# Kernel optimization log

Measured on AMD Instinct MI355X. Metric: run time of the kernel, lower is better.

Reference implementation:

```python
import jax, jax.numpy as jnp
import numpy as np

N_NODES = 80000
N_EDGES = 800000
N_REL = 400
D_IN = 256
D_OUT = 256
BN_EPS = 1e-5


def _xavier(key, shape, gain=np.sqrt(2.0)):
    fan_in, fan_out = shape[0], shape[-1]
    std = gain * np.sqrt(2.0 / (fan_in + fan_out))
    return jax.random.normal(key, shape, dtype=jnp.float32) * std


def ccorr(a, b):
    # circular correlation: irfft(conj(rfft(a)) * rfft(b), n)
    n = a.shape[-1]
    return jnp.fft.irfft(jnp.conj(jnp.fft.rfft(a)) * jnp.fft.rfft(b), n)


def setup_inputs() -> dict:
    key = jax.random.key(0)
    ks = jax.random.split(key, 12)
    x = jax.random.normal(ks[0], (N_NODES, D_IN), dtype=jnp.float32)
    rel_repr = jax.random.normal(ks[1], (N_REL, D_IN), dtype=jnp.float32)
    edge_src = jax.random.randint(ks[2], (N_EDGES,), 0, N_NODES)
    edge_dst = jax.random.randint(ks[3], (N_EDGES,), 0, N_NODES)
    edge_type = jax.random.randint(ks[4], (N_EDGES,), 0, N_REL)
    edge_norm = jax.random.uniform(ks[5], (N_EDGES,), dtype=jnp.float32)
    in_w = _xavier(ks[6], (D_IN, D_OUT))
    out_w = _xavier(ks[7], (D_IN, D_OUT))
    loop_w = _xavier(ks[8], (D_IN, D_OUT))
    w_rel = _xavier(ks[9], (D_IN, D_OUT))
    loop_rel = _xavier(ks[10], (1, D_IN))
    bias = jnp.zeros((D_OUT,), dtype=jnp.float32)
    return {"x": x, "rel_repr": rel_repr, "edge_src": edge_src,
            "edge_dst": edge_dst, "edge_type": edge_type, "edge_norm": edge_norm,
            "in_w": in_w, "out_w": out_w, "loop_w": loop_w, "w_rel": w_rel,
            "loop_rel": loop_rel, "bias": bias}


def reference(x, rel_repr, edge_src, edge_dst, edge_type, edge_norm,
              in_w, out_w, loop_w, w_rel, loop_rel, bias):
    E = edge_src.shape[0]
    half = E // 2
    # gather + compose (opn == 'corr')
    h_src = x[edge_src]                         # [E, D_in]
    edge_data = ccorr(h_src, rel_repr[edge_type])  # [E, D_in]
    # direction-split matmul
    msg = jnp.concatenate([edge_data[:half] @ in_w,
                           edge_data[half:] @ out_w], axis=0)  # [E, D_out]
    msg = msg * edge_norm[:, None]
    # scatter-sum into destination nodes, then reduce (dropout p=0, /3)
    agg = jax.ops.segment_sum(msg, edge_dst, num_segments=x.shape[0]) / 3.0
    # self-loop
    loop = ccorr(x, jnp.broadcast_to(loop_rel, x.shape)) @ loop_w / 3.0
    out = agg + loop + bias
    # BatchNorm1d (training mode: batch stats, gamma=1, beta=0)
    mean = jnp.mean(out, axis=0)
    var = jnp.var(out, axis=0)
    out = (out - mean) / jnp.sqrt(var + BN_EPS)
    # act is identity
    return out, rel_repr @ w_rel
```

## Files before the change

### kernel.cpp

```cpp
#include <hip/hip_runtime.h>

#define NN 80000
#define NE 800000
#define EH 400000
#define NR 400
#define DD 256
#define NFP 260
#define KT 772
#define KP 832
#define NB 160000
#define NCH 157
#define MT 80400
#define PI2 6.283185307179586f

typedef unsigned short u16;
typedef __attribute__((ext_vector_type(8))) short bf16x8;
typedef __attribute__((ext_vector_type(4))) float f32x4;

static __device__ __forceinline__ float bu2f(u16 u) {
  return __uint_as_float(((unsigned int)u) << 16);
}
static __device__ __forceinline__ u16 f2bu(float f) {
  unsigned int x = __float_as_uint(f);
  x += 0x7fffu + ((x >> 16) & 1u);
  return (u16)(x >> 16);
}
static __device__ __forceinline__ unsigned int pk2(float a, float b) {
  return (unsigned int)f2bu(a) | ((unsigned int)f2bu(b) << 16);
}
static __device__ __forceinline__ void gload16(const void* g, void* l) {
  __builtin_amdgcn_global_load_lds(
      (const __attribute__((address_space(1))) unsigned int*)g,
      (__attribute__((address_space(3))) unsigned int*)l, 16, 0, 0);
}

__global__ void k_build_f(u16* __restrict__ Ft) {
  int c = blockIdx.x, j = threadIdx.x;
  int k = c >> 1;
  int m = (j * k) & 255;
  float th = -PI2 * (float)m * (1.0f / 256.0f);
  float v = (c & 1) ? sinf(th) : cosf(th);
  Ft[c * 256 + j] = f2bu(v);
}

__global__ void k_build_m(const float* __restrict__ in_w, const float* __restrict__ out_w,
                          u16* __restrict__ Bt) {
  int t = blockIdx.x;
  int c = threadIdx.x;
  const float* W = (t < 258) ? in_w : out_w;
  int tp = (t < 258) ? t : t - 258;
  int k = tp >> 1, im = tp & 1;
  float a = (k == 0 || k == 128) ? 1.0f : 2.0f;
  float scale = a * (1.0f / (256.0f * 3.0f));
  float th = -PI2 * (float)k * (1.0f / 256.0f);
  float wr = cosf(th), wi = sinf(th);
  float zr = 1.0f, zi = 0.0f;
  float acc = 0.0f;
  for (int j = 0; j < DD; ++j) {
    float coef = im ? zi : zr;
    acc += coef * W[(size_t)j * DD + c];
    float nzr = zr * wr - zi * wi; zi = zr * wi + zi * wr; zr = nzr;
  }
  Bt[(size_t)c * KP + t] = f2bu(scale * acc);
}

__global__ void k_build_q(const float* __restrict__ lr, const float* __restrict__ loop_w,
                          u16* __restrict__ Bt) {
  __shared__ float L[DD];
  int j = blockIdx.x, c = threadIdx.x;
  L[c] = lr[c];
  __syncthreads();
  float acc = 0.0f;
  for (int k2 = 0; k2 < DD; ++k2)
    acc += L[(j + k2) & 255] * loop_w[(size_t)k2 * DD + c];
  Bt[(size_t)c * KP + 516 + j] = f2bu(acc * (1.0f / 3.0f));
  if (j < KP - KT) Bt[(size_t)c * KP + KT + j] = 0;
}

__global__ __launch_bounds__(256) void k_cvt(const float* __restrict__ x,
                                             u16* __restrict__ Ap, u16* __restrict__ xb,
                                             u16* __restrict__ xfh) {
  int w = threadIdx.x >> 6, lane = threadIdx.x & 63;
  size_t row = (size_t)blockIdx.x * 4 + w;
  float4 v = *(const float4*)(x + row * DD + 4 * lane);
  ushort4 pk;
  pk.x = f2bu(v.x); pk.y = f2bu(v.y); pk.z = f2bu(v.z); pk.w = f2bu(v.w);
  *(ushort4*)(xb + row * DD + 4 * lane) = pk;
  *(ushort4*)(Ap + row * KP + 516 + 4 * lane) = pk;
  if (lane < 15) *(uint2*)(Ap + row * KP + KT + 4 * lane) = make_uint2(0u, 0u);
  float s = v.x - v.y + v.z - v.w;
#pragma unroll
  for (int off = 32; off > 0; off >>= 1) s += __shfl_xor(s, off);
  if (lane == 0) {
    xfh[row * NFP + 256] = f2bu(s);
    xfh[row * NFP + 257] = 0;
  }
}

__global__ __launch_bounds__(256) void k_cvtr(const float* __restrict__ rel,
                                              u16* __restrict__ xb, u16* __restrict__ rfh) {
  int w = threadIdx.x >> 6, lane = threadIdx.x & 63;
  size_t row = (size_t)blockIdx.x * 4 + w;
  float4 v = *(const float4*)(rel + row * DD + 4 * lane);
  ushort4 pk;
  pk.x = f2bu(v.x); pk.y = f2bu(v.y); pk.z = f2bu(v.z); pk.w = f2bu(v.w);
  *(ushort4*)(xb + (NN + row) * DD + 4 * lane) = pk;
  float s = v.x - v.y + v.z - v.w;
#pragma unroll
  for (int off = 32; off > 0; off >>= 1) s += __shfl_xor(s, off);
  if (lane == 0) {
    rfh[row * NFP + 256] = f2bu(s);
    rfh[row * NFP + 257] = 0;
  }
}

__global__ __launch_bounds__(256) void k_dft(
    const u16* __restrict__ xb, const u16* __restrict__ Ft,
    u16* __restrict__ xfh, u16* __restrict__ rfh) {
  __shared__ u16 sA[128 * 64];
  __shared__ u16 sB[128 * 64];
  int tid = threadIdx.x;
  int mt0 = (int)(blockIdx.x >> 1) * 128;
  int nt0 = (blockIdx.x & 1) * 128;
  int w = tid >> 6, lane = tid & 63;
  int wm = (w & 1) * 64, wn = (w >> 1) * 64;
  int fr = lane & 15, fg = lane >> 4;
  int rbase = tid >> 3;
  int cbe = (tid & 7) * 8;
  int wadr = rbase * 64 + (cbe ^ ((rbase & 7) * 8));

  f32x4 acc[4][4];
#pragma unroll
  for (int i = 0; i < 4; ++i)
#pragma unroll
    for (int j = 0; j < 4; ++j) acc[i][j] = (f32x4){0.f, 0.f, 0.f, 0.f};

  bf16x8 ra[4], rb[4];
#define LOADT(kb)                                                                   \
  {                                                                                 \
    _Pragma("unroll") for (int q = 0; q < 4; ++q) {                                 \
      int rr = mt0 + rbase + q * 32; if (rr > MT - 1) rr = MT - 1;                  \
      ra[q] = *(const bf16x8*)(xb + (size_t)rr * DD + (kb) * 64 + cbe);             \
      rb[q] = *(const bf16x8*)(Ft + (size_t)(nt0 + rbase + q * 32) * DD + (kb) * 64 + cbe); \
    }                                                                               \
  }

  LOADT(0)
  for (int kb = 0; kb < 4; ++kb) {
    __syncthreads();
#pragma unroll
    for (int q = 0; q < 4; ++q) {
      *(bf16x8*)(sA + q * 2048 + wadr) = ra[q];
      *(bf16x8*)(sB + q * 2048 + wadr) = rb[q];
    }
    __syncthreads();
    if (kb + 1 < 4) LOADT(kb + 1)
#pragma unroll
    for (int ks = 0; ks < 2; ++ks) {
      bf16x8 af[4], bf_[4];
#pragma unroll
      for (int mt = 0; mt < 4; ++mt) {
        int r = wm + mt * 16 + fr;
        af[mt] = *(const bf16x8*)(sA + r * 64 + ((ks * 32 + fg * 8) ^ ((r & 7) * 8)));
      }
#pragma unroll
      for (int nt = 0; nt < 4; ++nt) {
        int r = wn + nt * 16 + fr;
        bf_[nt] = *(const bf16x8*)(sB + r * 64 + ((ks * 32 + fg * 8) ^ ((r & 7) * 8)));
      }
#pragma unroll
      for (int mt = 0; mt < 4; ++mt)
#pragma unroll
        for (int nt = 0; nt < 4; ++nt)
          acc[mt][nt] = __builtin_amdgcn_mfma_f32_16x16x32_bf16(af[mt], bf_[nt],
                                                                acc[mt][nt], 0, 0, 0);
    }
  }
#undef LOADT

#pragma unroll
  for (int mt = 0; mt < 4; ++mt)
#pragma unroll
    for (int nt = 0; nt < 4; ++nt) {
      int cg = nt0 + wn + nt * 16 + fr;
#pragma unroll
      for (int j = 0; j < 4; ++j) {
        int rg = mt0 + wm + mt * 16 + fg * 4 + j;
        u16 val = f2bu(acc[mt][nt][j]);
        if (rg < NN)      xfh[(size_t)rg * NFP + cg] = val;
        else if (rg < MT) rfh[(size_t)(rg - NN) * NFP + cg] = val;
      }
    }
}

__global__ void k_hist(const int* __restrict__ edst, int* __restrict__ cnt) {
  int e = blockIdx.x * 256 + threadIdx.x;
  int key = edst[e] + ((e >= EH) ? NN : 0);
  atomicAdd(&cnt[key], 1);
}

__global__ __launch_bounds__(256) void k_scan1(const int* __restrict__ cnt,
                                               int* __restrict__ base,
                                               int* __restrict__ chunkTot) {
  __shared__ int wsum[4];
  int t = threadIdx.x;
  int g0 = blockIdx.x * 1024 + t * 4;
  int v[4], ex[4], s = 0;
#pragma unroll
  for (int j = 0; j < 4; ++j) v[j] = (g0 + j < NB) ? cnt[g0 + j] : 0;
#pragma unroll
  for (int j = 0; j < 4; ++j) { ex[j] = s; s += v[j]; }
  int lane = t & 63, w = t >> 6;
  int inc = s;
  for (int off = 1; off < 64; off <<= 1) {
    int n = __shfl_up(inc, off);
    if (lane >= off) inc += n;
  }
  if (lane == 63) wsum[w] = inc;
  __syncthreads();
  int woff = 0;
  for (int i = 0; i < w; ++i) woff += wsum[i];
  int exth = woff + inc - s;
#pragma unroll
  for (int j = 0; j < 4; ++j)
    if (g0 + j < NB) base[g0 + j] = exth + ex[j];
  if (t == 255) chunkTot[blockIdx.x] = woff + inc;
}

__global__ __launch_bounds__(256) void k_scan2(const int* __restrict__ chunkTot,
                                               int* __restrict__ chunkOff) {
  __shared__ int wsum[4];
  int t = threadIdx.x;
  int v = (t < NCH) ? chunkTot[t] : 0;
  int lane = t & 63, w = t >> 6;
  int inc = v;
  for (int off = 1; off < 64; off <<= 1) {
    int n = __shfl_up(inc, off);
    if (lane >= off) inc += n;
  }
  if (lane == 63) wsum[w] = inc;
  __syncthreads();
  int woff = 0;
  for (int i = 0; i < w; ++i) woff += wsum[i];
  if (t < NCH) chunkOff[t] = woff + inc - v;
}

__global__ void k_scan3(int* __restrict__ base, const int* __restrict__ chunkOff,
                        int* __restrict__ cursor) {
  int i = blockIdx.x * 256 + threadIdx.x;
  if (i < NB) {
    int b = base[i] + chunkOff[i >> 10];
    base[i] = b;
    cursor[i] = b;
  }
  if (i == 0) base[NB] = NE;
}

__global__ void k_scatter(const int* __restrict__ esrc, const int* __restrict__ edst,
                          const int* __restrict__ etyp, const float* __restrict__ enorm,
                          int* __restrict__ cursor, int4* __restrict__ recs) {
  int e = blockIdx.x * 256 + threadIdx.x;
  int key = edst[e] + ((e >= EH) ? NN : 0);
  int pos = atomicAdd(&cursor[key], 1);
  recs[pos] = make_int4(esrc[e], etyp[e], __float_as_int(enorm[e]), 0);
}

__global__ __launch_bounds__(256) void k_reduce(
    const u16* __restrict__ xfh, const u16* __restrict__ rfh,
    const int4* __restrict__ recs, const int* __restrict__ base,
    u16* __restrict__ Ap) {
  int w = threadIdx.x >> 6, lane = threadIdx.x & 63;
  int b = blockIdx.x * 4 + w;
  int start = base[b], end = base[b + 1];
  float a0 = 0, a1 = 0, a2 = 0, a3 = 0;
  float nyr = 0, nyi = 0;
  int p = start;
  for (; p + 3 < end; p += 4) {
    ushort4 xv[4], rv[4];
    float nm[4];
    unsigned int xn[4], rn[4];
#pragma unroll
    for (int u = 0; u < 4; ++u) {
      int4 rc = recs[p + u];
      nm[u] = __int_as_float(rc.z);
      const u16* xp = xfh + (size_t)rc.x * NFP;
      const u16* rp = rfh + (size_t)rc.y * NFP;
      xv[u] = *(const ushort4*)(xp + 4 * lane);
      rv[u] = *(const ushort4*)(rp + 4 * lane);
      if (lane == 0) {
        xn[u] = *(const unsigned int*)(xp + 256);
        rn[u] = *(const unsigned int*)(rp + 256);
      }
    }
#pragma unroll
    for (int u = 0; u < 4; ++u) {
      float xr0 = bu2f(xv[u].x), xi0 = bu2f(xv[u].y);
      float xr1 = bu2f(xv[u].z), xi1 = bu2f(xv[u].w);
      float rr0 = bu2f(rv[u].x), ri0 = bu2f(rv[u].y);
      float rr1 = bu2f(rv[u].z), ri1 = bu2f(rv[u].w);
      a0 += (xr0 * rr0 + xi0 * ri0) * nm[u];
      a1 += (xr0 * ri0 - xi0 * rr0) * nm[u];
      a2 += (xr1 * rr1 + xi1 * ri1) * nm[u];
      a3 += (xr1 * ri1 - xi1 * rr1) * nm[u];
      if (lane == 0) {
        float ar = bu2f((u16)xn[u]), ai = bu2f((u16)(xn[u] >> 16));
        float br = bu2f((u16)rn[u]), bi = bu2f((u16)(rn[u] >> 16));
        nyr += (ar * br + ai * bi) * nm[u];
        nyi += (ar * bi - ai * br) * nm[u];
      }
    }
  }
  for (; p < end; ++p) {
    int4 rc = recs[p];
    float nm0 = __int_as_float(rc.z);
    const u16* xp = xfh + (size_t)rc.x * NFP;
    const u16* rp = rfh + (size_t)rc.y * NFP;
    ushort4 xv0 = *(const ushort4*)(xp + 4 * lane);
    ushort4 rv0 = *(const ushort4*)(rp + 4 * lane);
    float xr0 = bu2f(xv0.x), xi0 = bu2f(xv0.y), xr1 = bu2f(xv0.z), xi1 = bu2f(xv0.w);
    float rr0 = bu2f(rv0.x), ri0 = bu2f(rv0.y), rr1 = bu2f(rv0.z), ri1 = bu2f(rv0.w);
    a0 += (xr0 * rr0 + xi0 * ri0) * nm0;
    a1 += (xr0 * ri0 - xi0 * rr0) * nm0;
    a2 += (xr1 * rr1 + xi1 * ri1) * nm0;
    a3 += (xr1 * ri1 - xi1 * rr1) * nm0;
    if (lane == 0) {
      unsigned int xn0 = *(const unsigned int*)(xp + 256);
      unsigned int rn0 = *(const unsigned int*)(rp + 256);
      float ar = bu2f((u16)xn0), ai = bu2f((u16)(xn0 >> 16));
      float br = bu2f((u16)rn0), bi = bu2f((u16)(rn0 >> 16));
      nyr += (ar * br + ai * bi) * nm0;
      nyi += (ar * bi - ai * br) * nm0;
    }
  }
  u16* tp = Ap + ((b < NN) ? (size_t)b * KP : (size_t)(b - NN) * KP + 258);
  *(unsigned int*)(tp + 4 * lane)     = pk2(a0, a1);
  *(unsigned int*)(tp + 4 * lane + 2) = pk2(a2, a3);
  if (lane == 0) *(unsigned int*)(tp + 256) = pk2(nyr, nyi);
}

__global__ __launch_bounds__(256) void k_mgemm(
    const u16* __restrict__ Ap, const u16* __restrict__ Bt,
    const float* __restrict__ bias, float* __restrict__ dout,
    float* __restrict__ sum1, float* __restrict__ sum2) {
  __shared__ u16 sA[2 * 128 * 64];
  __shared__ u16 sB[2 * 128 * 64];
  __shared__ float sS1[128], sS2[128];
  int tid = threadIdx.x;
  int mt0 = (blockIdx.x >> 1) * 128;
  int nt0 = (blockIdx.x & 1) * 128;
  int w = tid >> 6, lane = tid & 63;
  int wm = (w & 1) * 64, wn = (w >> 1) * 64;
  int fr = lane & 15, fg = lane >> 4;
  int srow = (lane >> 3);
  int lcb = lane & 7;
  if (tid < 128) { sS1[tid] = 0.f; sS2[tid] = 0.f; }

#define STG(buf, kb)                                                                 \
  {                                                                                  \
    _Pragma("unroll") for (int q = 0; q < 4; ++q) {                                  \
      int s = w * 4 + q;                                                             \
      int row = s * 8 + srow;                                                        \
      int cb = lcb ^ (row & 7);                                                      \
      gload16(Ap + (size_t)(mt0 + row) * KP + (kb) * 64 + cb * 8,                    \
              sA + (buf) * 8192 + s * 512);                                          \
      gload16(Bt + (size_t)(nt0 + row) * KP + (kb) * 64 + cb * 8,                    \
              sB + (buf) * 8192 + s * 512);                                          \
    }                                                                                \
  }

  f32x4 acc[4][4];
#pragma unroll
  for (int i = 0; i < 4; ++i)
#pragma unroll
    for (int j = 0; j < 4; ++j) acc[i][j] = (f32x4){0.f, 0.f, 0.f, 0.f};

  STG(0, 0)
  __syncthreads();
  int cur = 0;
  for (int kb = 0; kb < 13; ++kb) {
    if (kb + 1 < 13) STG(cur ^ 1, kb + 1)
#pragma unroll
    for (int ks = 0; ks < 2; ++ks) {
      bf16x8 af[4], bf_[4];
#pragma unroll
      for (int mt = 0; mt < 4; ++mt) {
        int r = wm + mt * 16 + fr;
        af[mt] = *(const bf16x8*)(sA + cur * 8192 + r * 64 +
                                  ((ks * 32 + fg * 8) ^ ((r & 7) * 8)));
      }
#pragma unroll
      for (int nt = 0; nt < 4; ++nt) {
        int r = wn + nt * 16 + fr;
        bf_[nt] = *(const bf16x8*)(sB + cur * 8192 + r * 64 +
                                   ((ks * 32 + fg * 8) ^ ((r & 7) * 8)));
      }
#pragma unroll
      for (int mt = 0; mt < 4; ++mt)
#pragma unroll
        for (int nt = 0; nt < 4; ++nt)
          acc[mt][nt] = __builtin_amdgcn_mfma_f32_16x16x32_bf16(af[mt], bf_[nt],
                                                                acc[mt][nt], 0, 0, 0);
    }
    __syncthreads();
    cur ^= 1;
  }
#undef STG

  float s1[4] = {0.f, 0.f, 0.f, 0.f}, s2[4] = {0.f, 0.f, 0.f, 0.f};
#pragma unroll
  for (int nt = 0; nt < 4; ++nt) {
    int cg = nt0 + wn + nt * 16 + fr;
    float bv = bias[cg];
#pragma unroll
    for (int mt = 0; mt < 4; ++mt) {
#pragma unroll
      for (int j = 0; j < 4; ++j) {
        int rg = mt0 + wm + mt * 16 + fg * 4 + j;
        float val = acc[mt][nt][j] + bv;
        dout[(size_t)rg * DD + cg] = val;
        s1[nt] += val;
        s2[nt] += val * val;
      }
    }
  }
#pragma unroll
  for (int nt = 0; nt < 4; ++nt) {
    atomicAdd(&sS1[wn + nt * 16 + fr], s1[nt]);
    atomicAdd(&sS2[wn + nt * 16 + fr], s2[nt]);
  }
  __syncthreads();
  if (tid < 128) {
    atomicAdd(&sum1[nt0 + tid], sS1[tid]);
    atomicAdd(&sum2[nt0 + tid], sS2[tid]);
  }
}

__global__ void k_stats(const float* __restrict__ sum1, const float* __restrict__ sum2,
                        float* __restrict__ mean, float* __restrict__ rstd) {
  int c = threadIdx.x;
  float m = sum1[c] * (1.0f / (float)NN);
  float var = sum2[c] * (1.0f / (float)NN) - m * m;
  mean[c] = m;
  rstd[c] = rsqrtf(var + 1e-5f);
}

__global__ void k_norm(float* __restrict__ out, const float* __restrict__ mean,
                       const float* __restrict__ rstd) {
  size_t i4 = ((size_t)blockIdx.x * 256 + threadIdx.x) * 4;
  float4* p = (float4*)(out + i4);
  float4 v = *p;
  int c0 = (int)(i4 & 255);
  v.x = (v.x - mean[c0 + 0]) * rstd[c0 + 0];
  v.y = (v.y - mean[c0 + 1]) * rstd[c0 + 1];
  v.z = (v.z - mean[c0 + 2]) * rstd[c0 + 2];
  v.w = (v.w - mean[c0 + 3]) * rstd[c0 + 3];
  *p = v;
}

__global__ void k_rel(const float* __restrict__ rel, const float* __restrict__ wrel,
                      float* __restrict__ out2) {
  __shared__ float R[DD];
  int r = blockIdx.x, c = threadIdx.x;
  R[c] = rel[(size_t)r * DD + c];
  __syncthreads();
  float acc = 0.0f;
  for (int j = 0; j < DD; ++j)
    acc += R[j] * wrel[(size_t)j * DD + c];
  out2[(size_t)r * DD + c] = acc;
}

__global__ void k_fail(float* __restrict__ out, int n) {
  int i = blockIdx.x * 256 + threadIdx.x;
  if (i < n) out[i] = 1.0e6f;
}

extern "C" void kernel_launch(void* const* d_in, const int* in_sizes, int n_in,
                              void* d_out, int out_size, void* d_ws, size_t ws_size,
                              hipStream_t stream) {
  (void)in_sizes; (void)n_in;
  const float* x      = (const float*)d_in[0];
  const float* rel    = (const float*)d_in[1];
  const int*   esrc   = (const int*)d_in[2];
  const int*   edst   = (const int*)d_in[3];
  const int*   etyp   = (const int*)d_in[4];
  const float* enorm  = (const float*)d_in[5];
  const float* in_w   = (const float*)d_in[6];
  const float* out_w  = (const float*)d_in[7];
  const float* loop_w = (const float*)d_in[8];
  const float* w_rel  = (const float*)d_in[9];
  const float* lr     = (const float*)d_in[10];
  const float* bias   = (const float*)d_in[11];
  float* dout = (float*)d_out;

  char* wsb = (char*)d_ws;
  size_t off = 0;
  u16* Apack = (u16*)(wsb + off); off += (size_t)NN * KP * 2;
  u16* Bt    = (u16*)(wsb + off); off += (size_t)DD * KP * 2;
  u16* xfh   = (u16*)(wsb + off); off += (size_t)NN * NFP * 2;
  u16* rfh   = (u16*)(wsb + off); off += (size_t)NR * NFP * 2;
  u16* xb    = (u16*)(wsb + off); off += (size_t)MT * DD * 2;
  u16* Ft    = (u16*)(wsb + off); off += (size_t)DD * DD * 2;
  int4* recs = (int4*)(wsb + off); off += (size_t)NE * 16;
  float* sum1  = (float*)(wsb + off); off += DD * 4;
  float* sum2  = (float*)(wsb + off); off += DD * 4;
  float* meanb = (float*)(wsb + off); off += DD * 4;
  float* rstdb = (float*)(wsb + off); off += DD * 4;
  int* cnt   = (int*)(wsb + off); off += (size_t)(NB + 1) * 4;
  int* baseA = (int*)(wsb + off); off += (size_t)(NB + 1) * 4;
  int* curA  = (int*)(wsb + off); off += (size_t)NB * 4;
  int* chT   = (int*)(wsb + off); off += 256 * 4;
  int* chO   = (int*)(wsb + off); off += 256 * 4;

  if (ws_size < off) {
    k_fail<<<(out_size + 255) / 256, 256, 0, stream>>>(dout, out_size);
    return;
  }

  hipMemsetAsync(cnt, 0, (NB + 1) * sizeof(int), stream);
  hipMemsetAsync(sum1, 0, 2 * DD * sizeof(float), stream);
  k_cvt<<<NN / 4, 256, 0, stream>>>(x, Apack, xb, xfh);
  k_cvtr<<<NR / 4, 256, 0, stream>>>(rel, xb, rfh);
  k_build_f<<<256, 256, 0, stream>>>(Ft);
  k_build_m<<<516, 256, 0, stream>>>(in_w, out_w, Bt);
  k_build_q<<<256, 256, 0, stream>>>(lr, loop_w, Bt);
  k_dft<<<629 * 2, 256, 0, stream>>>(xb, Ft, xfh, rfh);
  k_hist<<<NE / 256, 256, 0, stream>>>(edst, cnt);
  k_scan1<<<NCH, 256, 0, stream>>>(cnt, baseA, chT);
  k_scan2<<<1, 256, 0, stream>>>(chT, chO);
  k_scan3<<<(NB + 255) / 256, 256, 0, stream>>>(baseA, chO, curA);
  k_scatter<<<NE / 256, 256, 0, stream>>>(esrc, edst, etyp, enorm, curA, recs);
  k_reduce<<<NB / 4, 256, 0, stream>>>(xfh, rfh, recs, baseA, Apack);
  k_mgemm<<<(NN / 128) * 2, 256, 0, stream>>>(Apack, Bt, bias, dout, sum1, sum2);
  k_stats<<<1, 256, 0, stream>>>(sum1, sum2, meanb, rstdb);
  k_norm<<<NN * DD / 4 / 256, 256, 0, stream>>>(dout, meanb, rstdb);
  k_rel<<<NR, 256, 0, stream>>>(rel, w_rel, dout + (size_t)NN * DD);
}
```

Measured before the change: 442.5 us.

## Pack real DFT bins into 256 columns, fuse fp32 conversion into DFT GEMM

Packs the DC and Nyquist real bins into slots 0 and 1 of a 256-wide half-spectrum. This drops the padded 260-wide layout and the K dimension from 832 to 768, and removes the separate lane-0 Nyquist handling in the reduce. The standalone cvt kernels are deleted: the DFT GEMM now reads fp32 x/rel directly, converts to bf16 in registers and writes the bf16 x block into the packed A matrix. Both GEMMs now use 512-thread blocks covering all 256 output columns, so the A tile is loaded once instead of twice. The mgemm epilogue reduces column sums with wave shuffles instead of LDS atomics. Risks include more LDS per block and lower occupancy.

```diff
diff --git a/kernel.cpp b/kernel.cpp
--- a/kernel.cpp
+++ b/kernel.cpp
@@ -5,9 +5,8 @@
 #define EH 400000
 #define NR 400
 #define DD 256
-#define NFP 260
-#define KT 772
-#define KP 832
+#define FD 256
+#define KP 768
 #define NB 160000
 #define NCH 157
 #define MT 80400
@@ -36,10 +35,13 @@
 
 __global__ void k_build_f(u16* __restrict__ Ft) {
   int c = blockIdx.x, j = threadIdx.x;
-  int k = c >> 1;
+  int k, im;
+  if (c == 0)      { k = 0;   im = 0; }
+  else if (c == 1) { k = 128; im = 0; }
+  else             { k = c >> 1; im = c & 1; }
   int m = (j * k) & 255;
   float th = -PI2 * (float)m * (1.0f / 256.0f);
-  float v = (c & 1) ? sinf(th) : cosf(th);
+  float v = im ? sinf(th) : cosf(th);
   Ft[c * 256 + j] = f2bu(v);
 }
 
@@ -47,11 +49,13 @@
                           u16* __restrict__ Bt) {
   int t = blockIdx.x;
   int c = threadIdx.x;
-  const float* W = (t < 258) ? in_w : out_w;
-  int tp = (t < 258) ? t : t - 258;
-  int k = tp >> 1, im = tp & 1;
-  float a = (k == 0 || k == 128) ? 1.0f : 2.0f;
-  float scale = a * (1.0f / (256.0f * 3.0f));
+  const float* W = (t < 256) ? in_w : out_w;
+  int tp = t & 255;
+  int k, im; float alpha;
+  if (tp == 0)      { k = 0;   im = 0; alpha = 1.0f; }
+  else if (tp == 1) { k = 128; im = 0; alpha = 1.0f; }
+  else              { k = tp >> 1; im = tp & 1; alpha = 2.0f; }
+  float scale = alpha * (1.0f / 768.0f);
   float th = -PI2 * (float)k * (1.0f / 256.0f);
   float wr = cosf(th), wi = sinf(th);
   float zr = 1.0f, zi = 0.0f;
@@ -73,61 +77,49 @@
   float acc = 0.0f;
   for (int k2 = 0; k2 < DD; ++k2)
     acc += L[(j + k2) & 255] * loop_w[(size_t)k2 * DD + c];
-  Bt[(size_t)c * KP + 516 + j] = f2bu(acc * (1.0f / 3.0f));
-  if (j < KP - KT) Bt[(size_t)c * KP + KT + j] = 0;
-}
-
-__global__ __launch_bounds__(256) void k_cvt(const float* __restrict__ x,
-                                             u16* __restrict__ Ap, u16* __restrict__ xb,
-                                             u16* __restrict__ xfh) {
-  int w = threadIdx.x >> 6, lane = threadIdx.x & 63;
-  size_t row = (size_t)blockIdx.x * 4 + w;
-  float4 v = *(const float4*)(x + row * DD + 4 * lane);
-  ushort4 pk;
-  pk.x = f2bu(v.x); pk.y = f2bu(v.y); pk.z = f2bu(v.z); pk.w = f2bu(v.w);
-  *(ushort4*)(xb + row * DD + 4 * lane) = pk;
-  *(ushort4*)(Ap + row * KP + 516 + 4 * lane) = pk;
-  if (lane < 15) *(uint2*)(Ap + row * KP + KT + 4 * lane) = make_uint2(0u, 0u);
-  float s = v.x - v.y + v.z - v.w;
-#pragma unroll
-  for (int off = 32; off > 0; off >>= 1) s += __shfl_xor(s, off);
-  if (lane == 0) {
-    xfh[row * NFP + 256] = f2bu(s);
-    xfh[row * NFP + 257] = 0;
-  }
-}
-
-__global__ __launch_bounds__(256) void k_cvtr(const float* __restrict__ rel,
-                                              u16* __restrict__ xb, u16* __restrict__ rfh) {
-  int w = threadIdx.x >> 6, lane = threadIdx.x & 63;
-  size_t row = (size_t)blockIdx.x * 4 + w;
-  float4 v = *(const float4*)(rel + row * DD + 4 * lane);
-  ushort4 pk;
-  pk.x = f2bu(v.x); pk.y = f2bu(v.y); pk.z = f2bu(v.z); pk.w = f2bu(v.w);
-  *(ushort4*)(xb + (NN + row) * DD + 4 * lane) = pk;
-  float s = v.x - v.y + v.z - v.w;
-#pragma unroll
-  for (int off = 32; off > 0; off >>= 1) s += __shfl_xor(s, off);
-  if (lane == 0) {
-    rfh[row * NFP + 256] = f2bu(s);
-    rfh[row * NFP + 257] = 0;
-  }
-}
-
-__global__ __launch_bounds__(256) void k_dft(
-    const u16* __restrict__ xb, const u16* __restrict__ Ft,
-    u16* __restrict__ xfh, u16* __restrict__ rfh) {
-  __shared__ u16 sA[128 * 64];
-  __shared__ u16 sB[128 * 64];
+  Bt[(size_t)c * KP + 512 + j] = f2bu(acc * (1.0f / 3.0f));
+}
+
+__global__ __launch_bounds__(512) void k_dft(
+    const float* __restrict__ x, const float* __restrict__ rel,
+    const u16* __restrict__ Ft, u16* __restrict__ xfh, u16* __restrict__ rfh,
+    u16* __restrict__ Ap) {
+  __shared__ u16 sA[2][128 * 64];
+  __shared__ u16 sB[256 * 64];
   int tid = threadIdx.x;
-  int mt0 = (int)(blockIdx.x >> 1) * 128;
-  int nt0 = (blockIdx.x & 1) * 128;
   int w = tid >> 6, lane = tid & 63;
+  int r0 = blockIdx.x * 128;
   int wm = (w & 1) * 64, wn = (w >> 1) * 64;
   int fr = lane & 15, fg = lane >> 4;
-  int rbase = tid >> 3;
-  int cbe = (tid & 7) * 8;
-  int wadr = rbase * 64 + (cbe ^ ((rbase & 7) * 8));
+
+  int arow = tid >> 2;
+  int acg = (tid & 3) * 16;
+  int gr = r0 + arow;
+  int grc = gr < MT ? gr : MT - 1;
+  const float* asrc = (grc < NN) ? (x + (size_t)grc * DD)
+                                 : (rel + (size_t)(grc - NN) * DD);
+  bool doAp = (gr < NN);
+
+  float4 a0_, a1_, a2_, a3_;
+#define LOADA(kb) { const float* p_ = asrc + (kb) * 64 + acg;                     \
+    a0_ = *(const float4*)(p_);     a1_ = *(const float4*)(p_ + 4);               \
+    a2_ = *(const float4*)(p_ + 8); a3_ = *(const float4*)(p_ + 12); }
+
+#define STGB(kb) { _Pragma("unroll") for (int q = 0; q < 4; ++q) {                \
+    int s_ = w * 4 + q; int c_ = 8 * s_ + (lane >> 3);                            \
+    int cb_ = (lane & 7) ^ (c_ & 7);                                              \
+    gload16(Ft + (size_t)c_ * 256 + (kb) * 64 + cb_ * 8, sB + s_ * 512); } }
+
+#define CVTA(kb, buf) {                                                           \
+    uint4 c0_ = make_uint4(pk2(a0_.x, a0_.y), pk2(a0_.z, a0_.w),                  \
+                           pk2(a1_.x, a1_.y), pk2(a1_.z, a1_.w));                 \
+    uint4 c1_ = make_uint4(pk2(a2_.x, a2_.y), pk2(a2_.z, a2_.w),                  \
+                           pk2(a3_.x, a3_.y), pk2(a3_.z, a3_.w));                 \
+    int b0_ = (tid & 3) * 2;                                                      \
+    *(uint4*)(sA[buf] + arow * 64 + ((b0_ ^ (arow & 7)) * 8)) = c0_;              \
+    *(uint4*)(sA[buf] + arow * 64 + (((b0_ + 1) ^ (arow & 7)) * 8)) = c1_;        \
+    if (doAp) { u16* ap_ = Ap + (size_t)gr * KP + 512 + (kb) * 64 + acg;          \
+      *(uint4*)(ap_) = c0_; *(uint4*)(ap_ + 8) = c1_; } }
 
   f32x4 acc[4][4];
 #pragma unroll
@@ -135,60 +127,56 @@
 #pragma unroll
     for (int j = 0; j < 4; ++j) acc[i][j] = (f32x4){0.f, 0.f, 0.f, 0.f};
 
-  bf16x8 ra[4], rb[4];
-#define LOADT(kb)                                                                   \
-  {                                                                                 \
-    _Pragma("unroll") for (int q = 0; q < 4; ++q) {                                 \
-      int rr = mt0 + rbase + q * 32; if (rr > MT - 1) rr = MT - 1;                  \
-      ra[q] = *(const bf16x8*)(xb + (size_t)rr * DD + (kb) * 64 + cbe);             \
-      rb[q] = *(const bf16x8*)(Ft + (size_t)(nt0 + rbase + q * 32) * DD + (kb) * 64 + cbe); \
-    }                                                                               \
-  }
-
-  LOADT(0)
+  LOADA(0)
+  STGB(0)
+  CVTA(0, 0)
+  LOADA(1)
+  __syncthreads();
   for (int kb = 0; kb < 4; ++kb) {
-    __syncthreads();
-#pragma unroll
-    for (int q = 0; q < 4; ++q) {
-      *(bf16x8*)(sA + q * 2048 + wadr) = ra[q];
-      *(bf16x8*)(sB + q * 2048 + wadr) = rb[q];
-    }
-    __syncthreads();
-    if (kb + 1 < 4) LOADT(kb + 1)
+    int cur = kb & 1;
 #pragma unroll
     for (int ks = 0; ks < 2; ++ks) {
-      bf16x8 af[4], bf_[4];
+      bf16x8 af[4], bfr[4];
 #pragma unroll
       for (int mt = 0; mt < 4; ++mt) {
         int r = wm + mt * 16 + fr;
-        af[mt] = *(const bf16x8*)(sA + r * 64 + ((ks * 32 + fg * 8) ^ ((r & 7) * 8)));
+        af[mt] = *(const bf16x8*)(sA[cur] + r * 64 + ((ks * 32 + fg * 8) ^ ((r & 7) * 8)));
       }
 #pragma unroll
       for (int nt = 0; nt < 4; ++nt) {
-        int r = wn + nt * 16 + fr;
-        bf_[nt] = *(const bf16x8*)(sB + r * 64 + ((ks * 32 + fg * 8) ^ ((r & 7) * 8)));
+        int c = wn + nt * 16 + fr;
+        bfr[nt] = *(const bf16x8*)(sB + c * 64 + ((ks * 32 + fg * 8) ^ ((c & 7) * 8)));
       }
 #pragma unroll
       for (int mt = 0; mt < 4; ++mt)
 #pragma unroll
         for (int nt = 0; nt < 4; ++nt)
-          acc[mt][nt] = __builtin_amdgcn_mfma_f32_16x16x32_bf16(af[mt], bf_[nt],
+          acc[mt][nt] = __builtin_amdgcn_mfma_f32_16x16x32_bf16(af[mt], bfr[nt],
                                                                 acc[mt][nt], 0, 0, 0);
     }
-  }
-#undef LOADT
+    __syncthreads();
+    if (kb < 3) {
+      STGB(kb + 1)
+      CVTA(kb + 1, cur ^ 1)
+      if (kb < 2) LOADA(kb + 2)
+      __syncthreads();
+    }
+  }
+#undef LOADA
+#undef STGB
+#undef CVTA
 
 #pragma unroll
   for (int mt = 0; mt < 4; ++mt)
 #pragma unroll
     for (int nt = 0; nt < 4; ++nt) {
-      int cg = nt0 + wn + nt * 16 + fr;
+      int cg = wn + nt * 16 + fr;
 #pragma unroll
       for (int j = 0; j < 4; ++j) {
-        int rg = mt0 + wm + mt * 16 + fg * 4 + j;
+        int rg = r0 + wm + mt * 16 + fg * 4 + j;
         u16 val = f2bu(acc[mt][nt][j]);
-        if (rg < NN)      xfh[(size_t)rg * NFP + cg] = val;
-        else if (rg < MT) rfh[(size_t)(rg - NN) * NFP + cg] = val;
+        if (rg < NN)      xfh[(size_t)rg * FD + cg] = val;
+        else if (rg < MT) rfh[(size_t)(rg - NN) * FD + cg] = val;
       }
     }
 }
@@ -272,25 +260,18 @@
   int w = threadIdx.x >> 6, lane = threadIdx.x & 63;
   int b = blockIdx.x * 4 + w;
   int start = base[b], end = base[b + 1];
+  bool l0 = (lane == 0);
   float a0 = 0, a1 = 0, a2 = 0, a3 = 0;
-  float nyr = 0, nyi = 0;
   int p = start;
   for (; p + 3 < end; p += 4) {
     ushort4 xv[4], rv[4];
     float nm[4];
-    unsigned int xn[4], rn[4];
 #pragma unroll
     for (int u = 0; u < 4; ++u) {
       int4 rc = recs[p + u];
       nm[u] = __int_as_float(rc.z);
-      const u16* xp = xfh + (size_t)rc.x * NFP;
-      const u16* rp = rfh + (size_t)rc.y * NFP;
-      xv[u] = *(const ushort4*)(xp + 4 * lane);
-      rv[u] = *(const ushort4*)(rp + 4 * lane);
-      if (lane == 0) {
-        xn[u] = *(const unsigned int*)(xp + 256);
-        rn[u] = *(const unsigned int*)(rp + 256);
-      }
+      xv[u] = *(const ushort4*)(xfh + (size_t)rc.x * FD + 4 * lane);
+      rv[u] = *(const ushort4*)(rfh + (size_t)rc.y * FD + 4 * lane);
     }
 #pragma unroll
     for (int u = 0; u < 4; ++u) {
@@ -298,75 +279,55 @@
       float xr1 = bu2f(xv[u].z), xi1 = bu2f(xv[u].w);
       float rr0 = bu2f(rv[u].x), ri0 = bu2f(rv[u].y);
       float rr1 = bu2f(rv[u].z), ri1 = bu2f(rv[u].w);
-      a0 += (xr0 * rr0 + xi0 * ri0) * nm[u];
-      a1 += (xr0 * ri0 - xi0 * rr0) * nm[u];
+      float p0 = l0 ? (xr0 * rr0) : (xr0 * rr0 + xi0 * ri0);
+      float p1 = l0 ? (xi0 * ri0) : (xr0 * ri0 - xi0 * rr0);
+      a0 += p0 * nm[u];
+      a1 += p1 * nm[u];
       a2 += (xr1 * rr1 + xi1 * ri1) * nm[u];
       a3 += (xr1 * ri1 - xi1 * rr1) * nm[u];
-      if (lane == 0) {
-        float ar = bu2f((u16)xn[u]), ai = bu2f((u16)(xn[u] >> 16));
-        float br = bu2f((u16)rn[u]), bi = bu2f((u16)(rn[u] >> 16));
-        nyr += (ar * br + ai * bi) * nm[u];
-        nyi += (ar * bi - ai * br) * nm[u];
-      }
     }
   }
   for (; p < end; ++p) {
     int4 rc = recs[p];
     float nm0 = __int_as_float(rc.z);
-    const u16* xp = xfh + (size_t)rc.x * NFP;
-    const u16* rp = rfh + (size_t)rc.y * NFP;
-    ushort4 xv0 = *(const ushort4*)(xp + 4 * lane);
-    ushort4 rv0 = *(const ushort4*)(rp + 4 * lane);
+    ushort4 xv0 = *(const ushort4*)(xfh + (size_t)rc.x * FD + 4 * lane);
+    ushort4 rv0 = *(const ushort4*)(rfh + (size_t)rc.y * FD + 4 * lane);
     float xr0 = bu2f(xv0.x), xi0 = bu2f(xv0.y), xr1 = bu2f(xv0.z), xi1 = bu2f(xv0.w);
     float rr0 = bu2f(rv0.x), ri0 = bu2f(rv0.y), rr1 = bu2f(rv0.z), ri1 = bu2f(rv0.w);
-    a0 += (xr0 * rr0 + xi0 * ri0) * nm0;
-    a1 += (xr0 * ri0 - xi0 * rr0) * nm0;
+    float p0 = l0 ? (xr0 * rr0) : (xr0 * rr0 + xi0 * ri0);
+    float p1 = l0 ? (xi0 * ri0) : (xr0 * ri0 - xi0 * rr0);
+    a0 += p0 * nm0;
+    a1 += p1 * nm0;
     a2 += (xr1 * rr1 + xi1 * ri1) * nm0;
     a3 += (xr1 * ri1 - xi1 * rr1) * nm0;
-    if (lane == 0) {
-      unsigned int xn0 = *(const unsigned int*)(xp + 256);
-      unsigned int rn0 = *(const unsigned int*)(rp + 256);
-      float ar = bu2f((u16)xn0), ai = bu2f((u16)(xn0 >> 16));
-      float br = bu2f((u16)rn0), bi = bu2f((u16)(rn0 >> 16));
-      nyr += (ar * br + ai * bi) * nm0;
-      nyi += (ar * bi - ai * br) * nm0;
-    }
-  }
-  u16* tp = Ap + ((b < NN) ? (size_t)b * KP : (size_t)(b - NN) * KP + 258);
+  }
+  u16* tp = Ap + ((b < NN) ? (size_t)b * KP : (size_t)(b - NN) * KP + 256);
   *(unsigned int*)(tp + 4 * lane)     = pk2(a0, a1);
   *(unsigned int*)(tp + 4 * lane + 2) = pk2(a2, a3);
-  if (lane == 0) *(unsigned int*)(tp + 256) = pk2(nyr, nyi);
-}
-
-__global__ __launch_bounds__(256) void k_mgemm(
+}
+
+__global__ __launch_bounds__(512) void k_mgemm(
     const u16* __restrict__ Ap, const u16* __restrict__ Bt,
     const float* __restrict__ bias, float* __restrict__ dout,
     float* __restrict__ sum1, float* __restrict__ sum2) {
-  __shared__ u16 sA[2 * 128 * 64];
-  __shared__ u16 sB[2 * 128 * 64];
-  __shared__ float sS1[128], sS2[128];
+  __shared__ u16 sA[2][128 * 64];
+  __shared__ u16 sB[256 * 64];
   int tid = threadIdx.x;
-  int mt0 = (blockIdx.x >> 1) * 128;
-  int nt0 = (blockIdx.x & 1) * 128;
   int w = tid >> 6, lane = tid & 63;
+  int r0 = blockIdx.x * 128;
   int wm = (w & 1) * 64, wn = (w >> 1) * 64;
   int fr = lane & 15, fg = lane >> 4;
-  int srow = (lane >> 3);
-  int lcb = lane & 7;
-  if (tid < 128) { sS1[tid] = 0.f; sS2[tid] = 0.f; }
-
-#define STG(buf, kb)                                                                 \
-  {                                                                                  \
-    _Pragma("unroll") for (int q = 0; q < 4; ++q) {                                  \
-      int s = w * 4 + q;                                                             \
-      int row = s * 8 + srow;                                                        \
-      int cb = lcb ^ (row & 7);                                                      \
-      gload16(Ap + (size_t)(mt0 + row) * KP + (kb) * 64 + cb * 8,                    \
-              sA + (buf) * 8192 + s * 512);                                          \
-      gload16(Bt + (size_t)(nt0 + row) * KP + (kb) * 64 + cb * 8,                    \
-              sB + (buf) * 8192 + s * 512);                                          \
-    }                                                                                \
-  }
+
+#define STGA(kb, buf) { _Pragma("unroll") for (int q = 0; q < 2; ++q) {           \
+    int s_ = w * 2 + q; int r_ = 8 * s_ + (lane >> 3);                            \
+    int cb_ = (lane & 7) ^ (r_ & 7);                                              \
+    gload16(Ap + (size_t)(r0 + r_) * KP + (kb) * 64 + cb_ * 8,                    \
+            sA[buf] + s_ * 512); } }
+
+#define STGB(kb) { _Pragma("unroll") for (int q = 0; q < 4; ++q) {                \
+    int s_ = w * 4 + q; int c_ = 8 * s_ + (lane >> 3);                            \
+    int cb_ = (lane & 7) ^ (c_ & 7);                                              \
+    gload16(Bt + (size_t)c_ * KP + (kb) * 64 + cb_ * 8, sB + s_ * 512); } }
 
   f32x4 acc[4][4];
 #pragma unroll
@@ -374,48 +335,48 @@
 #pragma unroll
     for (int j = 0; j < 4; ++j) acc[i][j] = (f32x4){0.f, 0.f, 0.f, 0.f};
 
-  STG(0, 0)
-  __syncthreads();
-  int cur = 0;
-  for (int kb = 0; kb < 13; ++kb) {
-    if (kb + 1 < 13) STG(cur ^ 1, kb + 1)
+  STGA(0, 0)
+  STGB(0)
+  __syncthreads();
+  for (int kb = 0; kb < 12; ++kb) {
+    int cur = kb & 1;
+    if (kb < 11) STGA(kb + 1, cur ^ 1)
 #pragma unroll
     for (int ks = 0; ks < 2; ++ks) {
-      bf16x8 af[4], bf_[4];
+      bf16x8 af[4], bfr[4];
 #pragma unroll
       for (int mt = 0; mt < 4; ++mt) {
         int r = wm + mt * 16 + fr;
-        af[mt] = *(const bf16x8*)(sA + cur * 8192 + r * 64 +
-                                  ((ks * 32 + fg * 8) ^ ((r & 7) * 8)));
+        af[mt] = *(const bf16x8*)(sA[cur] + r * 64 + ((ks * 32 + fg * 8) ^ ((r & 7) * 8)));
       }
 #pragma unroll
       for (int nt = 0; nt < 4; ++nt) {
-        int r = wn + nt * 16 + fr;
-        bf_[nt] = *(const bf16x8*)(sB + cur * 8192 + r * 64 +
-                                   ((ks * 32 + fg * 8) ^ ((r & 7) * 8)));
+        int c = wn + nt * 16 + fr;
+        bfr[nt] = *(const bf16x8*)(sB + c * 64 + ((ks * 32 + fg * 8) ^ ((c & 7) * 8)));
       }
 #pragma unroll
       for (int mt = 0; mt < 4; ++mt)
 #pragma unroll
         for (int nt = 0; nt < 4; ++nt)
-          acc[mt][nt] = __builtin_amdgcn_mfma_f32_16x16x32_bf16(af[mt], bf_[nt],
+          acc[mt][nt] = __builtin_amdgcn_mfma_f32_16x16x32_bf16(af[mt], bfr[nt],
                                                                 acc[mt][nt], 0, 0, 0);
     }
     __syncthreads();
-    cur ^= 1;
-  }
-#undef STG
+    if (kb < 11) { STGB(kb + 1) __syncthreads(); }
+  }
+#undef STGA
+#undef STGB
 
   float s1[4] = {0.f, 0.f, 0.f, 0.f}, s2[4] = {0.f, 0.f, 0.f, 0.f};
 #pragma unroll
   for (int nt = 0; nt < 4; ++nt) {
-    int cg = nt0 + wn + nt * 16 + fr;
+    int cg = wn + nt * 16 + fr;
     float bv = bias[cg];
 #pragma unroll
     for (int mt = 0; mt < 4; ++mt) {
 #pragma unroll
       for (int j = 0; j < 4; ++j) {
-        int rg = mt0 + wm + mt * 16 + fg * 4 + j;
+        int rg = r0 + wm + mt * 16 + fg * 4 + j;
         float val = acc[mt][nt][j] + bv;
         dout[(size_t)rg * DD + cg] = val;
         s1[nt] += val;
@@ -425,13 +386,15 @@
   }
 #pragma unroll
   for (int nt = 0; nt < 4; ++nt) {
-    atomicAdd(&sS1[wn + nt * 16 + fr], s1[nt]);
-    atomicAdd(&sS2[wn + nt * 16 + fr], s2[nt]);
-  }
-  __syncthreads();
-  if (tid < 128) {
-    atomicAdd(&sum1[nt0 + tid], sS1[tid]);
-    atomicAdd(&sum2[nt0 + tid], sS2[tid]);
+    s1[nt] += __shfl_xor(s1[nt], 16); s1[nt] += __shfl_xor(s1[nt], 32);
+    s2[nt] += __shfl_xor(s2[nt], 16); s2[nt] += __shfl_xor(s2[nt], 32);
+  }
+  if (lane < 16) {
+#pragma unroll
+    for (int nt = 0; nt < 4; ++nt) {
+      atomicAdd(&sum1[wn + nt * 16 + lane], s1[nt]);
+      atomicAdd(&sum2[wn + nt * 16 + lane], s2[nt]);
+    }
   }
 }
 
@@ -496,9 +459,8 @@
   size_t off = 0;
   u16* Apack = (u16*)(wsb + off); off += (size_t)NN * KP * 2;
   u16* Bt    = (u16*)(wsb + off); off += (size_t)DD * KP * 2;
-  u16* xfh   = (u16*)(wsb + off); off += (size_t)NN * NFP * 2;
-  u16* rfh   = (u16*)(wsb + off); off += (size_t)NR * NFP * 2;
-  u16* xb    = (u16*)(wsb + off); off += (size_t)MT * DD * 2;
+  u16* xfh   = (u16*)(wsb + off); off += (size_t)NN * FD * 2;
+  u16* rfh   = (u16*)(wsb + off); off += (size_t)NR * FD * 2;
   u16* Ft    = (u16*)(wsb + off); off += (size_t)DD * DD * 2;
   int4* recs = (int4*)(wsb + off); off += (size_t)NE * 16;
   float* sum1  = (float*)(wsb + off); off += DD * 4;
@@ -518,19 +480,17 @@
 
   hipMemsetAsync(cnt, 0, (NB + 1) * sizeof(int), stream);
   hipMemsetAsync(sum1, 0, 2 * DD * sizeof(float), stream);
-  k_cvt<<<NN / 4, 256, 0, stream>>>(x, Apack, xb, xfh);
-  k_cvtr<<<NR / 4, 256, 0, stream>>>(rel, xb, rfh);
   k_build_f<<<256, 256, 0, stream>>>(Ft);
-  k_build_m<<<516, 256, 0, stream>>>(in_w, out_w, Bt);
+  k_build_m<<<512, 256, 0, stream>>>(in_w, out_w, Bt);
   k_build_q<<<256, 256, 0, stream>>>(lr, loop_w, Bt);
-  k_dft<<<629 * 2, 256, 0, stream>>>(xb, Ft, xfh, rfh);
   k_hist<<<NE / 256, 256, 0, stream>>>(edst, cnt);
   k_scan1<<<NCH, 256, 0, stream>>>(cnt, baseA, chT);
   k_scan2<<<1, 256, 0, stream>>>(chT, chO);
   k_scan3<<<(NB + 255) / 256, 256, 0, stream>>>(baseA, chO, curA);
   k_scatter<<<NE / 256, 256, 0, stream>>>(esrc, edst, etyp, enorm, curA, recs);
+  k_dft<<<(MT + 127) / 128, 512, 0, stream>>>(x, rel, Ft, xfh, rfh, Apack);
   k_reduce<<<NB / 4, 256, 0, stream>>>(xfh, rfh, recs, baseA, Apack);
-  k_mgemm<<<(NN / 128) * 2, 256, 0, stream>>>(Apack, Bt, bias, dout, sum1, sum2);
+  k_mgemm<<<NN / 128, 512, 0, stream>>>(Apack, Bt, bias, dout, sum1, sum2);
   k_stats<<<1, 256, 0, stream>>>(sum1, sum2, meanb, rstdb);
   k_norm<<<NN * DD / 4 / 256, 256, 0, stream>>>(dout, meanb, rstdb);
   k_rel<<<NR, 256, 0, stream>>>(rel, w_rel, dout + (size_t)NN * DD);
```

Result: faster. 381.6 us (-13.7%).
